# Kernel optimization log

Hardware: AMD Instinct MI355X
Metric: run time of the kernel (lower is better)

The kernel has to match this reference:

```python
import jax, jax.numpy as jnp
import numpy as np

OUT_NPOINT = 1024
NSAMPLE = 64
RADIUS = 0.32
BN_EPS = 1e-5


def _fps_single(pts, npoint):
    # pts: [N,3] -> indices [npoint], sequential furthest point sampling (starts at index 0,
    # matching pointnet2's furthest_point_sample with dists initialized to 1e10).
    N = pts.shape[0]

    def step(carry, _):
        mind, last = carry
        d = jnp.sum((pts - pts[last]) ** 2, axis=-1)  # [N]
        mind = jnp.minimum(mind, d)
        nxt = jnp.argmax(mind).astype(jnp.int32)
        return (mind, nxt), last

    init = (jnp.full((N,), 1e10, dtype=pts.dtype), jnp.int32(0))
    (_, _), idxs = jax.lax.scan(step, init, None, length=npoint)
    return idxs  # [npoint]


def _ball_query(xyz, new_xyz, radius, nsample):
    # xyz: [B,N,3], new_xyz: [B,M,3] -> idx [B,M,nsample] (first nsample in-ball points,
    # padded with the first found index, matching pointnet2 ball_query semantics).
    N = xyz.shape[1]
    d2 = jnp.sum((new_xyz[:, :, None, :] - xyz[:, None, :, :]) ** 2, axis=-1)  # [B,M,N]
    inball = d2 < radius * radius
    key = jnp.where(inball, jnp.arange(N, dtype=jnp.int32)[None, None, :], jnp.int32(N))
    sorted_keys = jnp.sort(key, axis=-1)[..., :nsample]  # [B,M,nsample]
    valid = sorted_keys < N
    first = jnp.where(sorted_keys[..., 0:1] < N, sorted_keys[..., 0:1], 0)
    return jnp.where(valid, sorted_keys, first)


def _group(features, idx):
    # features: [B,C,N], idx: [B,M,S] -> [B,C,M,S]
    return jax.vmap(lambda f, i: f[:, i])(features, idx)


def setup_inputs() -> dict:
    key = jax.random.key(0)
    ks = jax.random.split(key, 8)
    B, N, Cin, Cout = 8, 4096, 128, 256
    xyz = jax.random.uniform(ks[0], (B, N, 3), dtype=jnp.float32)
    features = jax.random.normal(ks[1], (B, Cin, N), dtype=jnp.float32)
    W = jax.random.normal(ks[2], (Cout, Cin), dtype=jnp.float32) * 0.05  # 1x1 conv weight
    b = jax.random.normal(ks[3], (Cout,), dtype=jnp.float32) * 0.05
    gamma = jax.random.uniform(ks[4], (Cout,), minval=0.5, maxval=1.5, dtype=jnp.float32)
    beta = jax.random.normal(ks[5], (Cout,), dtype=jnp.float32) * 0.1
    run_mean = jax.random.normal(ks[6], (Cout,), dtype=jnp.float32) * 0.1
    run_var = jax.random.uniform(ks[7], (Cout,), minval=0.5, maxval=1.5, dtype=jnp.float32)
    return {"xyz": xyz, "features": features, "W": W, "b": b,
            "gamma": gamma, "beta": beta, "run_mean": run_mean, "run_var": run_var}


def reference(xyz, features, W, b, gamma, beta, run_mean, run_var):
    # FPS to pick OUT_NPOINT centers
    fps_idx = jax.vmap(lambda p: _fps_single(p, OUT_NPOINT))(xyz)          # [B,M]
    new_xyz = jnp.take_along_axis(xyz, fps_idx[:, :, None], axis=1)        # [B,M,3]
    # ball-query neighbor indices and gather features (use_xyz=False)
    idx = _ball_query(xyz, new_xyz, RADIUS, NSAMPLE)                        # [B,M,S]
    grouped = _group(features, idx)                                         # [B,Cin,M,S]
    # pointwise conv (1x1) + BN (inference mode) + ReLU
    out = jnp.einsum('oc,bcms->boms', W, grouped) + b[None, :, None, None]  # [B,Cout,M,S]
    inv = jax.lax.rsqrt(run_var + BN_EPS)
    out = (out - run_mean[None, :, None, None]) * (gamma * inv)[None, :, None, None] + beta[None, :, None, None]
    out = jax.nn.relu(out)
    # max-pool over the neighbor axis
    return jnp.max(out, axis=-1)  # [B,Cout,M]
```

## Files before the change

### kernel.cpp

```cpp
#include <hip/hip_runtime.h>

#define N_PTS 4096
#define B_SZ  8
#define M_OUT 1024
#define NS    64
#define CIN   128
#define COUT  256

typedef float v2f __attribute__((ext_vector_type(2)));

__device__ __forceinline__ float dpp_max_f32(float v) {
  int x = __builtin_bit_cast(int, v);
#define STG(C)                                                              \
  {                                                                         \
    int y = __builtin_amdgcn_update_dpp(x, x, C, 0xF, 0xF, false);          \
    float a = __builtin_bit_cast(float, x);                                 \
    float b2 = __builtin_bit_cast(float, y);                                \
    a = fmaxf(a, b2);                                                       \
    x = __builtin_bit_cast(int, a);                                         \
  }
  STG(0x111) STG(0x112) STG(0x114) STG(0x118) STG(0x142) STG(0x143)
#undef STG
  return __builtin_bit_cast(float, __builtin_amdgcn_readlane(x, 63));
}

__global__ __launch_bounds__(256) void fps_conv_kernel(
    const float* __restrict__ xyz, int* __restrict__ fps_idx,
    const float* __restrict__ F, const float* __restrict__ W,
    float* __restrict__ Z) {
  __shared__ __align__(16) float smem[13360];
  if (blockIdx.x < 8) {
#pragma clang fp contract(off)
    float* lx = smem;
    float* ly = smem + 4096;
    float* lz = smem + 8192;
    float4 (*sl)[4] = (float4(*)[4])(smem + 12288);
    int (*siw)[4] = (int(*)[4])(smem + 12320);
    int* wlds = (int*)(smem + 12328);
    const int b = blockIdx.x, t = threadIdx.x;
    const int lane = t & 63, wv = t >> 6;
    const float* base = xyz + b * N_PTS * 3;
    for (int e = t; e < N_PTS; e += 256) {
      lx[e] = base[e * 3 + 0];
      ly[e] = base[e * 3 + 1];
      lz[e] = base[e * 3 + 2];
    }
    __syncthreads();
    const int nb = t * 16;
    v2f px[8], py[8], pz[8], m2[8];
#pragma unroll
    for (int j = 0; j < 8; ++j) {
      int n0 = nb + 2 * j;
      px[j] = (v2f){lx[n0], lx[n0 + 1]};
      py[j] = (v2f){ly[n0], ly[n0 + 1]};
      pz[j] = (v2f){lz[n0], lz[n0 + 1]};
      m2[j] = (v2f){1e10f, 1e10f};
    }
    int cur = 0;
    float cx = lx[0], cy = ly[0], cz = lz[0];
    for (int i = 0; i < M_OUT; ++i) {
      if (t == 0) wlds[i] = cur;
      float bv = -1.0f;
      int bj = 0;
#pragma unroll
      for (int j = 0; j < 8; ++j) {
        v2f dx = px[j] - cx, dy = py[j] - cy, dz = pz[j] - cz;
        v2f d = dx * dx + dy * dy;
        d = d + dz * dz;
        v2f md = __builtin_elementwise_min(m2[j], d);
        m2[j] = md;
        if (md.x > bv) { bv = md.x; bj = 2 * j; }
        if (md.y > bv) { bv = md.y; bj = 2 * j + 1; }
      }
      const float mv = dpp_max_f32(bv);
      unsigned long long tied = __ballot(bv == mv);
      const int fl = __ffsll(tied) - 1;
      const int bi = nb + bj;
      const int widx = __builtin_amdgcn_readlane(bi, fl);
      const float wx = lx[widx], wy = ly[widx], wz = lz[widx];
      const int p = i & 1;
      if (lane == 0) {
        sl[p][wv] = make_float4(mv, wx, wy, wz);
        siw[p][wv] = widx;
      }
      __syncthreads();
      float4 s0 = sl[p][0], s1 = sl[p][1], s2 = sl[p][2], s3 = sl[p][3];
      int i0 = siw[p][0], i1 = siw[p][1], i2 = siw[p][2], i3 = siw[p][3];
      float gv = s0.x, gx = s0.y, gy = s0.z, gz = s0.w;
      int gi = i0;
      bool bt;
      bt = (s1.x > gv) || (s1.x == gv && i1 < gi);
      if (bt) { gv = s1.x; gi = i1; gx = s1.y; gy = s1.z; gz = s1.w; }
      bt = (s2.x > gv) || (s2.x == gv && i2 < gi);
      if (bt) { gv = s2.x; gi = i2; gx = s2.y; gy = s2.z; gz = s2.w; }
      bt = (s3.x > gv) || (s3.x == gv && i3 < gi);
      if (bt) { gv = s3.x; gi = i3; gx = s3.y; gy = s3.z; gz = s3.w; }
      cur = gi; cx = gx; cy = gy; cz = gz;
    }
    __syncthreads();
    for (int e = t; e < M_OUT; e += 256) fps_idx[b * M_OUT + e] = wlds[e];
  } else {
    float (*Bs)[68] = (float(*)[68])smem;
    float (*As)[68] = (float(*)[68])(smem + 8704);
    const int bid = blockIdx.x - 8;
    const int n0 = (bid & 63) * 64;
    const int o0 = ((bid >> 6) & 3) * 64;
    const int b = bid >> 8;
    const int tid = threadIdx.x;
    for (int l = 0; l < 32; ++l) {
      int e = l * 256 + tid;
      int c = e & 127, oo = e >> 7;
      Bs[c][oo] = W[(o0 + oo) * CIN + c];
    }
    float acc[4][4] = {};
    const int tx = tid & 15, ty = tid >> 4;
    const float* Fb = F + b * CIN * N_PTS;
    for (int c0 = 0; c0 < CIN; c0 += 32) {
      __syncthreads();
      for (int l = 0; l < 8; ++l) {
        int e = l * 256 + tid;
        int nn = e & 63, cc = e >> 6;
        As[cc][nn] = Fb[(c0 + cc) * N_PTS + n0 + nn];
      }
      __syncthreads();
#pragma unroll
      for (int cc = 0; cc < 32; ++cc) {
        float4 a = *(const float4*)&As[cc][tx * 4];
        float4 w4 = *(const float4*)&Bs[c0 + cc][ty * 4];
        acc[0][0] += a.x * w4.x; acc[0][1] += a.x * w4.y; acc[0][2] += a.x * w4.z; acc[0][3] += a.x * w4.w;
        acc[1][0] += a.y * w4.x; acc[1][1] += a.y * w4.y; acc[1][2] += a.y * w4.z; acc[1][3] += a.y * w4.w;
        acc[2][0] += a.z * w4.x; acc[2][1] += a.z * w4.y; acc[2][2] += a.z * w4.z; acc[2][3] += a.z * w4.w;
        acc[3][0] += a.w * w4.x; acc[3][1] += a.w * w4.y; acc[3][2] += a.w * w4.z; acc[3][3] += a.w * w4.w;
      }
    }
    float* Zb = Z + (size_t)(b * N_PTS + n0) * COUT + o0;
#pragma unroll
    for (int i = 0; i < 4; ++i) {
      int nn = tx * 4 + i;
      float4 v = make_float4(acc[i][0], acc[i][1], acc[i][2], acc[i][3]);
      *(float4*)&Zb[(size_t)nn * COUT + ty * 4] = v;
    }
  }
}

__global__ __launch_bounds__(512) void ballq_pool_kernel(
    const float* __restrict__ xyz, const int* __restrict__ fps_idx,
    const float* __restrict__ Z, const float* __restrict__ bias,
    const float* __restrict__ gamma, const float* __restrict__ beta,
    const float* __restrict__ rmean, const float* __restrict__ rvar,
    float* __restrict__ out) {
  __shared__ float T[COUT][9];
  __shared__ __align__(16) int sidx[8 * NS];
  const int b = blockIdx.x & 7;
  const int m0 = (blockIdx.x >> 3) * 8;
  const int lane = threadIdx.x & 63, wv = threadIdx.x >> 6;
  const float* base = xyz + b * N_PTS * 3;
  {
#pragma clang fp contract(off)
    const int cidx = fps_idx[b * M_OUT + m0 + wv];
    const float cx = base[cidx * 3 + 0], cy = base[cidx * 3 + 1],
                cz = base[cidx * 3 + 2];
    int* srow = sidx + wv * NS;
    int cnt = 0, first = 0;
    for (int ch = 0; ch < N_PTS / 64 && cnt < NS; ++ch) {
      const int n = ch * 64 + lane;
      float dx = base[n * 3 + 0] - cx;
      float dy = base[n * 3 + 1] - cy;
      float dz = base[n * 3 + 2] - cz;
      float d = dx * dx + dy * dy;
      d = d + dz * dz;
      const bool inb = d < 0.1024f;
      unsigned long long mask = __ballot(inb);
      if (cnt == 0 && mask) first = ch * 64 + (__ffsll(mask) - 1);
      const int pos = cnt + __popcll(mask & ((1ull << lane) - 1ull));
      if (inb && pos < NS) srow[pos] = n;
      cnt += (int)__popcll(mask);
    }
    if (lane >= cnt) srow[lane] = first;
  }
  __syncthreads();
  const int o = threadIdx.x & 255;
  const int half = threadIdx.x >> 8;
  const float sc = gamma[o] * (1.0f / sqrtf(rvar[o] + 1e-5f));
  const float bo = bias[o], mo = rmean[o], bt = beta[o];
  const float* Zb = Z + (size_t)b * N_PTS * COUT;
  for (int k = 0; k < 4; ++k) {
    const int mi = 2 * k + half;
    float c0 = -1e30f, c1 = -1e30f, c2 = -1e30f, c3 = -1e30f;
    float c4 = -1e30f, c5 = -1e30f, c6 = -1e30f, c7 = -1e30f;
#pragma unroll
    for (int s = 0; s < NS; s += 8) {
      int4 iv0 = *(const int4*)&sidx[mi * NS + s];
      int4 iv1 = *(const int4*)&sidx[mi * NS + s + 4];
      c0 = fmaxf(c0, Zb[(size_t)iv0.x * COUT + o]);
      c1 = fmaxf(c1, Zb[(size_t)iv0.y * COUT + o]);
      c2 = fmaxf(c2, Zb[(size_t)iv0.z * COUT + o]);
      c3 = fmaxf(c3, Zb[(size_t)iv0.w * COUT + o]);
      c4 = fmaxf(c4, Zb[(size_t)iv1.x * COUT + o]);
      c5 = fmaxf(c5, Zb[(size_t)iv1.y * COUT + o]);
      c6 = fmaxf(c6, Zb[(size_t)iv1.z * COUT + o]);
      c7 = fmaxf(c7, Zb[(size_t)iv1.w * COUT + o]);
    }
    float best = fmaxf(fmaxf(fmaxf(c0, c1), fmaxf(c2, c3)),
                       fmaxf(fmaxf(c4, c5), fmaxf(c6, c7)));
    float t = best + bo;
    t = (t - mo) * sc + bt;
    T[o][mi] = fmaxf(t, 0.0f);
  }
  __syncthreads();
  for (int l = 0; l < 4; ++l) {
    int e = l * 512 + (int)threadIdx.x;
    int mm = e & 7, oo = e >> 3;
    out[(size_t)(b * COUT + oo) * M_OUT + m0 + mm] = T[oo][mm];
  }
}

extern "C" void kernel_launch(void* const* d_in, const int* in_sizes, int n_in,
                              void* d_out, int out_size, void* d_ws, size_t ws_size,
                              hipStream_t stream) {
  const float* xyz      = (const float*)d_in[0];
  const float* features = (const float*)d_in[1];
  const float* W        = (const float*)d_in[2];
  const float* bias     = (const float*)d_in[3];
  const float* gamma    = (const float*)d_in[4];
  const float* beta     = (const float*)d_in[5];
  const float* rmean    = (const float*)d_in[6];
  const float* rvar     = (const float*)d_in[7];
  float* out = (float*)d_out;

  char* ws = (char*)d_ws;
  int* fps  = (int*)ws;
  float* Z  = (float*)(ws + (64 << 10) + (2 << 20));

  fps_conv_kernel<<<8 + 2048, 256, 0, stream>>>(xyz, fps, features, W, Z);
  ballq_pool_kernel<<<B_SZ * (M_OUT / 8), 512, 0, stream>>>(
      xyz, fps, Z, bias, gamma, beta, rmean, rvar, out);
}
```

Measured before the change: 839.2 us.

## Fuse FPS, conv and ball-query pooling into one persistent kernel with progress flags

Combines the two launches into a single persistent kernel. Eight blocks run FPS at raised priority and publish their indices in chunks of 64 through a per-batch progress counter. The remaining 496 worker blocks loop over the conv tiles, then meet at a global counter barrier, then run ball query and pooling per 8-center tile, spinning until the FPS counter covers that tile. The aim is to overlap the serial FPS phase with the pooling work and drop a launch boundary. In exchange it relies on all blocks being co-resident, since it uses spin-waits, and it adds a memset and atomics.

Result: slower. 874.4 us (+4.2%).

```diff
diff --git a/kernel.cpp b/kernel.cpp
--- a/kernel.cpp
+++ b/kernel.cpp
@@ -6,6 +6,7 @@
 #define NS    64
 #define CIN   128
 #define COUT  256
+#define NW    496
 
 typedef float v2f __attribute__((ext_vector_type(2)));
 
@@ -24,13 +25,18 @@
   return __builtin_bit_cast(float, __builtin_amdgcn_readlane(x, 63));
 }
 
-__global__ __launch_bounds__(256) void fps_conv_kernel(
+__global__ __launch_bounds__(256) void fused_kernel(
     const float* __restrict__ xyz, int* __restrict__ fps_idx,
+    int* __restrict__ gprog, int* __restrict__ gdone,
     const float* __restrict__ F, const float* __restrict__ W,
-    float* __restrict__ Z) {
+    float* __restrict__ Z, const float* __restrict__ bias,
+    const float* __restrict__ gamma, const float* __restrict__ beta,
+    const float* __restrict__ rmean, const float* __restrict__ rvar,
+    float* __restrict__ out) {
   __shared__ __align__(16) float smem[13360];
   if (blockIdx.x < 8) {
 #pragma clang fp contract(off)
+    __builtin_amdgcn_s_setprio(3);
     float* lx = smem;
     float* ly = smem + 4096;
     float* lz = smem + 8192;
@@ -96,122 +102,144 @@
       bt = (s3.x > gv) || (s3.x == gv && i3 < gi);
       if (bt) { gv = s3.x; gi = i3; gx = s3.y; gy = s3.z; gz = s3.w; }
       cur = gi; cx = gx; cy = gy; cz = gz;
+      if ((i & 63) == 63 && wv == 0) {
+        const int cb = i & ~63;
+        fps_idx[b * M_OUT + cb + lane] = wlds[cb + lane];
+        if (lane == 0)
+          __hip_atomic_store(gprog + b, i + 1, __ATOMIC_RELEASE,
+                             __HIP_MEMORY_SCOPE_AGENT);
+      }
+    }
+  } else {
+    const int w = blockIdx.x - 8;
+    {
+      float (*Bs)[68] = (float(*)[68])smem;
+      float (*As)[68] = (float(*)[68])(smem + 8704);
+      const int tid = threadIdx.x;
+      const int tx = tid & 15, ty = tid >> 4;
+      for (int tile = w; tile < 2048; tile += NW) {
+        __syncthreads();
+        const int n0 = (tile & 63) * 64;
+        const int o0 = ((tile >> 6) & 3) * 64;
+        const int bb = tile >> 8;
+        for (int l = 0; l < 32; ++l) {
+          int e = l * 256 + tid;
+          int c = e & 127, oo = e >> 7;
+          Bs[c][oo] = W[(o0 + oo) * CIN + c];
+        }
+        float acc[4][4] = {};
+        const float* Fb = F + bb * CIN * N_PTS;
+        for (int c0 = 0; c0 < CIN; c0 += 32) {
+          __syncthreads();
+          for (int l = 0; l < 8; ++l) {
+            int e = l * 256 + tid;
+            int nn = e & 63, cc = e >> 6;
+            As[cc][nn] = Fb[(c0 + cc) * N_PTS + n0 + nn];
+          }
+          __syncthreads();
+#pragma unroll
+          for (int cc = 0; cc < 32; ++cc) {
+            float4 a = *(const float4*)&As[cc][tx * 4];
+            float4 w4 = *(const float4*)&Bs[c0 + cc][ty * 4];
+            acc[0][0] += a.x * w4.x; acc[0][1] += a.x * w4.y; acc[0][2] += a.x * w4.z; acc[0][3] += a.x * w4.w;
+            acc[1][0] += a.y * w4.x; acc[1][1] += a.y * w4.y; acc[1][2] += a.y * w4.z; acc[1][3] += a.y * w4.w;
+            acc[2][0] += a.z * w4.x; acc[2][1] += a.z * w4.y; acc[2][2] += a.z * w4.z; acc[2][3] += a.z * w4.w;
+            acc[3][0] += a.w * w4.x; acc[3][1] += a.w * w4.y; acc[3][2] += a.w * w4.z; acc[3][3] += a.w * w4.w;
+          }
+        }
+        float* Zb = Z + (size_t)(bb * N_PTS + n0) * COUT + o0;
+#pragma unroll
+        for (int i2 = 0; i2 < 4; ++i2) {
+          int nn = tx * 4 + i2;
+          float4 v = make_float4(acc[i2][0], acc[i2][1], acc[i2][2], acc[i2][3]);
+          *(float4*)&Zb[(size_t)nn * COUT + ty * 4] = v;
+        }
+      }
     }
     __syncthreads();
-    for (int e = t; e < M_OUT; e += 256) fps_idx[b * M_OUT + e] = wlds[e];
-  } else {
-    float (*Bs)[68] = (float(*)[68])smem;
-    float (*As)[68] = (float(*)[68])(smem + 8704);
-    const int bid = blockIdx.x - 8;
-    const int n0 = (bid & 63) * 64;
-    const int o0 = ((bid >> 6) & 3) * 64;
-    const int b = bid >> 8;
-    const int tid = threadIdx.x;
-    for (int l = 0; l < 32; ++l) {
-      int e = l * 256 + tid;
-      int c = e & 127, oo = e >> 7;
-      Bs[c][oo] = W[(o0 + oo) * CIN + c];
-    }
-    float acc[4][4] = {};
-    const int tx = tid & 15, ty = tid >> 4;
-    const float* Fb = F + b * CIN * N_PTS;
-    for (int c0 = 0; c0 < CIN; c0 += 32) {
+    if (threadIdx.x == 0)
+      __hip_atomic_fetch_add(gdone, 1, __ATOMIC_RELEASE,
+                             __HIP_MEMORY_SCOPE_AGENT);
+    if (threadIdx.x == 0) {
+      while (__hip_atomic_load(gdone, __ATOMIC_ACQUIRE,
+                               __HIP_MEMORY_SCOPE_AGENT) < NW)
+        __builtin_amdgcn_s_sleep(16);
+    }
+    __syncthreads();
+    __builtin_amdgcn_fence(__ATOMIC_ACQUIRE, "agent");
+    const int lane = threadIdx.x & 63, wv = threadIdx.x >> 6;
+    const int o = threadIdx.x;
+    const float sc = gamma[o] * (1.0f / sqrtf(rvar[o] + 1e-5f));
+    const float bo = bias[o], mo = rmean[o], bt = beta[o];
+    float (*T)[9] = (float(*)[9])smem;
+    int* sidx = (int*)(smem + 2304);
+    for (int tb = w; tb < 1024; tb += NW) {
+      const int b = tb & 7;
+      const int m0 = (tb >> 3) * 8;
+      if (threadIdx.x == 0) {
+        while (__hip_atomic_load(gprog + b, __ATOMIC_ACQUIRE,
+                                 __HIP_MEMORY_SCOPE_AGENT) < m0 + 8)
+          __builtin_amdgcn_s_sleep(16);
+      }
+      __syncthreads();
+      __builtin_amdgcn_fence(__ATOMIC_ACQUIRE, "agent");
+      const float* base = xyz + b * N_PTS * 3;
+      {
+#pragma clang fp contract(off)
+        for (int c = wv; c < 8; c += 4) {
+          const int cidx = fps_idx[b * M_OUT + m0 + c];
+          const float cx = base[cidx * 3 + 0], cy = base[cidx * 3 + 1],
+                      cz = base[cidx * 3 + 2];
+          int* srow = sidx + c * NS;
+          int cnt = 0, first = 0;
+          for (int ch = 0; ch < N_PTS / 64 && cnt < NS; ++ch) {
+            const int n = ch * 64 + lane;
+            float dx = base[n * 3 + 0] - cx;
+            float dy = base[n * 3 + 1] - cy;
+            float dz = base[n * 3 + 2] - cz;
+            float d = dx * dx + dy * dy;
+            d = d + dz * dz;
+            const bool inb = d < 0.1024f;
+            unsigned long long mask = __ballot(inb);
+            if (cnt == 0 && mask) first = ch * 64 + (__ffsll(mask) - 1);
+            const int pos = cnt + __popcll(mask & ((1ull << lane) - 1ull));
+            if (inb && pos < NS) srow[pos] = n;
+            cnt += (int)__popcll(mask);
+          }
+          if (lane >= cnt) srow[lane] = first;
+        }
+      }
+      __syncthreads();
+      const float* Zb = Z + (size_t)b * N_PTS * COUT;
+      for (int mi = 0; mi < 8; ++mi) {
+        float c0 = -1e30f, c1 = -1e30f, c2 = -1e30f, c3 = -1e30f;
+        float c4 = -1e30f, c5 = -1e30f, c6 = -1e30f, c7 = -1e30f;
+#pragma unroll
+        for (int s = 0; s < NS; s += 8) {
+          int4 iv0 = *(const int4*)&sidx[mi * NS + s];
+          int4 iv1 = *(const int4*)&sidx[mi * NS + s + 4];
+          c0 = fmaxf(c0, Zb[(size_t)iv0.x * COUT + o]);
+          c1 = fmaxf(c1, Zb[(size_t)iv0.y * COUT + o]);
+          c2 = fmaxf(c2, Zb[(size_t)iv0.z * COUT + o]);
+          c3 = fmaxf(c3, Zb[(size_t)iv0.w * COUT + o]);
+          c4 = fmaxf(c4, Zb[(size_t)iv1.x * COUT + o]);
+          c5 = fmaxf(c5, Zb[(size_t)iv1.y * COUT + o]);
+          c6 = fmaxf(c6, Zb[(size_t)iv1.z * COUT + o]);
+          c7 = fmaxf(c7, Zb[(size_t)iv1.w * COUT + o]);
+        }
+        float best = fmaxf(fmaxf(fmaxf(c0, c1), fmaxf(c2, c3)),
+                           fmaxf(fmaxf(c4, c5), fmaxf(c6, c7)));
+        float tv = best + bo;
+        tv = (tv - mo) * sc + bt;
+        T[o][mi] = fmaxf(tv, 0.0f);
+      }
       __syncthreads();
       for (int l = 0; l < 8; ++l) {
-        int e = l * 256 + tid;
-        int nn = e & 63, cc = e >> 6;
-        As[cc][nn] = Fb[(c0 + cc) * N_PTS + n0 + nn];
-      }
-      __syncthreads();
-#pragma unroll
-      for (int cc = 0; cc < 32; ++cc) {
-        float4 a = *(const float4*)&As[cc][tx * 4];
-        float4 w4 = *(const float4*)&Bs[c0 + cc][ty * 4];
-        acc[0][0] += a.x * w4.x; acc[0][1] += a.x * w4.y; acc[0][2] += a.x * w4.z; acc[0][3] += a.x * w4.w;
-        acc[1][0] += a.y * w4.x; acc[1][1] += a.y * w4.y; acc[1][2] += a.y * w4.z; acc[1][3] += a.y * w4.w;
-        acc[2][0] += a.z * w4.x; acc[2][1] += a.z * w4.y; acc[2][2] += a.z * w4.z; acc[2][3] += a.z * w4.w;
-        acc[3][0] += a.w * w4.x; acc[3][1] += a.w * w4.y; acc[3][2] += a.w * w4.z; acc[3][3] += a.w * w4.w;
-      }
-    }
-    float* Zb = Z + (size_t)(b * N_PTS + n0) * COUT + o0;
-#pragma unroll
-    for (int i = 0; i < 4; ++i) {
-      int nn = tx * 4 + i;
-      float4 v = make_float4(acc[i][0], acc[i][1], acc[i][2], acc[i][3]);
-      *(float4*)&Zb[(size_t)nn * COUT + ty * 4] = v;
-    }
-  }
-}
-
-__global__ __launch_bounds__(512) void ballq_pool_kernel(
-    const float* __restrict__ xyz, const int* __restrict__ fps_idx,
-    const float* __restrict__ Z, const float* __restrict__ bias,
-    const float* __restrict__ gamma, const float* __restrict__ beta,
-    const float* __restrict__ rmean, const float* __restrict__ rvar,
-    float* __restrict__ out) {
-  __shared__ float T[COUT][9];
-  __shared__ __align__(16) int sidx[8 * NS];
-  const int b = blockIdx.x & 7;
-  const int m0 = (blockIdx.x >> 3) * 8;
-  const int lane = threadIdx.x & 63, wv = threadIdx.x >> 6;
-  const float* base = xyz + b * N_PTS * 3;
-  {
-#pragma clang fp contract(off)
-    const int cidx = fps_idx[b * M_OUT + m0 + wv];
-    const float cx = base[cidx * 3 + 0], cy = base[cidx * 3 + 1],
-                cz = base[cidx * 3 + 2];
-    int* srow = sidx + wv * NS;
-    int cnt = 0, first = 0;
-    for (int ch = 0; ch < N_PTS / 64 && cnt < NS; ++ch) {
-      const int n = ch * 64 + lane;
-      float dx = base[n * 3 + 0] - cx;
-      float dy = base[n * 3 + 1] - cy;
-      float dz = base[n * 3 + 2] - cz;
-      float d = dx * dx + dy * dy;
-      d = d + dz * dz;
-      const bool inb = d < 0.1024f;
-      unsigned long long mask = __ballot(inb);
-      if (cnt == 0 && mask) first = ch * 64 + (__ffsll(mask) - 1);
-      const int pos = cnt + __popcll(mask & ((1ull << lane) - 1ull));
-      if (inb && pos < NS) srow[pos] = n;
-      cnt += (int)__popcll(mask);
-    }
-    if (lane >= cnt) srow[lane] = first;
-  }
-  __syncthreads();
-  const int o = threadIdx.x & 255;
-  const int half = threadIdx.x >> 8;
-  const float sc = gamma[o] * (1.0f / sqrtf(rvar[o] + 1e-5f));
-  const float bo = bias[o], mo = rmean[o], bt = beta[o];
-  const float* Zb = Z + (size_t)b * N_PTS * COUT;
-  for (int k = 0; k < 4; ++k) {
-    const int mi = 2 * k + half;
-    float c0 = -1e30f, c1 = -1e30f, c2 = -1e30f, c3 = -1e30f;
-    float c4 = -1e30f, c5 = -1e30f, c6 = -1e30f, c7 = -1e30f;
-#pragma unroll
-    for (int s = 0; s < NS; s += 8) {
-      int4 iv0 = *(const int4*)&sidx[mi * NS + s];
-      int4 iv1 = *(const int4*)&sidx[mi * NS + s + 4];
-      c0 = fmaxf(c0, Zb[(size_t)iv0.x * COUT + o]);
-      c1 = fmaxf(c1, Zb[(size_t)iv0.y * COUT + o]);
-      c2 = fmaxf(c2, Zb[(size_t)iv0.z * COUT + o]);
-      c3 = fmaxf(c3, Zb[(size_t)iv0.w * COUT + o]);
-      c4 = fmaxf(c4, Zb[(size_t)iv1.x * COUT + o]);
-      c5 = fmaxf(c5, Zb[(size_t)iv1.y * COUT + o]);
-      c6 = fmaxf(c6, Zb[(size_t)iv1.z * COUT + o]);
-      c7 = fmaxf(c7, Zb[(size_t)iv1.w * COUT + o]);
-    }
-    float best = fmaxf(fmaxf(fmaxf(c0, c1), fmaxf(c2, c3)),
-                       fmaxf(fmaxf(c4, c5), fmaxf(c6, c7)));
-    float t = best + bo;
-    t = (t - mo) * sc + bt;
-    T[o][mi] = fmaxf(t, 0.0f);
-  }
-  __syncthreads();
-  for (int l = 0; l < 4; ++l) {
-    int e = l * 512 + (int)threadIdx.x;
-    int mm = e & 7, oo = e >> 3;
-    out[(size_t)(b * COUT + oo) * M_OUT + m0 + mm] = T[oo][mm];
+        int e = l * 256 + (int)threadIdx.x;
+        int mm = e & 7, oo = e >> 3;
+        out[(size_t)(b * COUT + oo) * M_OUT + m0 + mm] = T[oo][mm];
+      }
+    }
   }
 }
 
@@ -229,10 +257,12 @@
   float* out = (float*)d_out;
 
   char* ws = (char*)d_ws;
-  int* fps  = (int*)ws;
-  float* Z  = (float*)(ws + (64 << 10) + (2 << 20));
-
-  fps_conv_kernel<<<8 + 2048, 256, 0, stream>>>(xyz, fps, features, W, Z);
-  ballq_pool_kernel<<<B_SZ * (M_OUT / 8), 512, 0, stream>>>(
-      xyz, fps, Z, bias, gamma, beta, rmean, rvar, out);
+  int* fps   = (int*)ws;
+  int* flags = (int*)(ws + (48 << 10));
+  float* Z   = (float*)(ws + (64 << 10) + (2 << 20));
+
+  hipMemsetAsync(flags, 0, 64, stream);
+  fused_kernel<<<8 + NW, 256, 0, stream>>>(
+      xyz, fps, flags, flags + 8, features, W, Z, bias, gamma, beta, rmean,
+      rvar, out);
 }
```
